# Kernel optimization log

Hardware: AMD Instinct MI355X
Metric: run time of the kernel (lower is better)

Reference implementation:

```python
import jax, jax.numpy as jnp
import numpy as np

B, T, N_IN, N_H, N_OUT = 128, 1024, 512, 1024, 256


def setup_inputs() -> dict:
    key = jax.random.key(0)
    ks = jax.random.split(key, 14)
    s_in = 1.0 / np.sqrt(N_IN)
    s_h = 1.0 / np.sqrt(N_H)
    d = {
        'u': jax.random.normal(ks[0], (B, T, N_IN), jnp.float32),
        'W_uf': jax.random.normal(ks[1], (N_IN, N_H), jnp.float32) * s_in,
        'W_ui': jax.random.normal(ks[2], (N_IN, N_H), jnp.float32) * s_in,
        'W_uo': jax.random.normal(ks[3], (N_IN, N_H), jnp.float32) * s_in,
        'W_uc': jax.random.normal(ks[4], (N_IN, N_H), jnp.float32) * s_in,
        'W_hf': jax.random.normal(ks[5], (N_H, N_H), jnp.float32) * s_h,
        'W_hi': jax.random.normal(ks[6], (N_H, N_H), jnp.float32) * s_h,
        'W_ho': jax.random.normal(ks[7], (N_H, N_H), jnp.float32) * s_h,
        'W_hc': jax.random.normal(ks[8], (N_H, N_H), jnp.float32) * s_h,
        'W_hy': jax.random.normal(ks[9], (N_H, N_OUT), jnp.float32) * s_h,
        'b_f': jnp.zeros((N_H,), jnp.float32),
        'b_i': jnp.zeros((N_H,), jnp.float32),
        'b_o': jnp.zeros((N_H,), jnp.float32),
        'b_c': jnp.zeros((N_H,), jnp.float32),
        'b_y': jnp.zeros((N_OUT,), jnp.float32),
        'h0': jax.random.normal(ks[10], (N_H,), jnp.float32),
        'c0': jax.random.normal(ks[11], (N_H,), jnp.float32),
    }
    return d


def _lstm_forward(u, W_uf, W_ui, W_uo, W_uc, W_hf, W_hi, W_ho, W_hc, W_hy,
                  b_f, b_i, b_o, b_c, b_y, h0, c0):
    Bsz = u.shape[0]
    # Precompute all input-driven gate pre-activations as one batched GEMM per gate.
    xf = jnp.einsum('btn,nh->bth', u, W_uf) + b_f
    xi = jnp.einsum('btn,nh->bth', u, W_ui) + b_i
    xo = jnp.einsum('btn,nh->bth', u, W_uo) + b_o
    xc = jnp.einsum('btn,nh->bth', u, W_uc) + b_c
    xs = jnp.stack([xf, xi, xo, xc], axis=0)  # [4, B, T, H]
    xs = jnp.moveaxis(xs, 2, 0)               # [T, 4, B, H]

    h = jnp.broadcast_to(h0, (Bsz, h0.shape[0]))
    c = jnp.broadcast_to(c0, (Bsz, c0.shape[0]))

    def step(carry, x_t):
        h, c = carry
        f = jax.nn.sigmoid(h @ W_hf + x_t[0])
        i = jax.nn.sigmoid(h @ W_hi + x_t[1])
        o = jax.nn.sigmoid(h @ W_ho + x_t[2])
        c_tilde = jnp.tanh(h @ W_hc + x_t[3])
        # NOTE: faithful to source: c = f * h + i * c_tilde (uses h, not c)
        c_new = f * h + i * c_tilde
        h_new = o * jnp.tanh(c_new)
        y_t = jax.nn.softmax(h_new @ W_hy + b_y, axis=1)
        return (h_new, c_new), y_t

    (_, _), ys = jax.lax.scan(step, (h, c), xs)  # ys: [T, B, N_out]
    return jnp.swapaxes(ys, 0, 1)                # [B, T, N_out]


def reference(u, W_uf, W_ui, W_uo, W_uc, W_hf, W_hi, W_ho, W_hc, W_hy,
              b_f, b_i, b_o, b_c, b_y, h0, c0):
    return _lstm_forward(u, W_uf, W_ui, W_uo, W_uc, W_hf, W_hi, W_ho, W_hc,
                         W_hy, b_f, b_i, b_o, b_c, b_y, h0, c0)
```

## Files before the change

### kernel.cpp

```cpp
#include <hip/hip_runtime.h>
#include <hip/hip_bf16.h>
#include <hip/hip_cooperative_groups.h>

namespace cg = cooperative_groups;

#define BDIM 128
#define TDIM 1024
#define NIN  512
#define NH   1024
#define NOUT 256
#define NITER (TDIM + 2)

__device__ __forceinline__ float sigmoidf_(float x) { return 1.f / (1.f + __expf(-x)); }

struct ScanArgs {
    const float* u;
    const float* Wu[4];
    const float* Wh[4];
    const float* WhyT;
    const float* bg[4];
    const float* by;
    float* hb0; float* hb1;
    float* lg0; float* lg1;
    float* out;
};

__device__ __forceinline__ void scan_iter(const ScanArgs& A, int it,
                                          float* pre, float* ylds)
{
    const int tid  = threadIdx.x;
    const int bx   = blockIdx.x;
    const int lane = tid & 63;
    const int wv   = tid >> 6;
    const int ks   = lane & 7;
    const int cgi  = (lane >> 3) & 3;
    const int rg   = wv * 2 + (lane >> 5);
    const int c0   = bx * 4;

    const float* hcur = (it & 1) ? A.hb1 : A.hb0;
    float* hnext      = (it & 1) ? A.hb0 : A.hb1;
    float* Lw         = (it & 1) ? A.lg1 : A.lg0;
    const float* Lr   = (it & 1) ? A.lg0 : A.lg1;

    if (it >= 2 && bx < BDIM && tid < 64) {
        const int r = bx, t = it - 2;
        float4 v = *(const float4*)(Lr + (size_t)r * NOUT + tid * 4);
        float mx = fmaxf(fmaxf(v.x, v.y), fmaxf(v.z, v.w));
#pragma unroll
        for (int d = 1; d < 64; d <<= 1) mx = fmaxf(mx, __shfl_xor(mx, d));
        v.x = __expf(v.x - mx); v.y = __expf(v.y - mx);
        v.z = __expf(v.z - mx); v.w = __expf(v.w - mx);
        float s = v.x + v.y + v.z + v.w;
#pragma unroll
        for (int d = 1; d < 64; d <<= 1) s += __shfl_xor(s, d);
        const float inv = 1.f / s;
        v.x *= inv; v.y *= inv; v.z *= inv; v.w *= inv;
        *(float4*)(A.out + ((size_t)r * TDIM + t) * NOUT + tid * 4) = v;
    }

    if (it < TDIM) {
        const int t  = it;
        const int r0 = rg * 8;
        const float* Wu = A.Wu[cgi] + c0;
        const float* Wh = A.Wh[cgi] + c0;
        float acc[8][4];
#pragma unroll
        for (int i = 0; i < 8; ++i)
#pragma unroll
            for (int j = 0; j < 4; ++j) acc[i][j] = 0.f;

        {
            const int kb = ks * 64;
#pragma unroll 2
            for (int q = 0; q < 16; ++q) {
                const int k = kb + q * 4;
                const float4 w0 = *(const float4*)(Wu + (size_t)(k + 0) * NH);
                const float4 w1 = *(const float4*)(Wu + (size_t)(k + 1) * NH);
                const float4 w2 = *(const float4*)(Wu + (size_t)(k + 2) * NH);
                const float4 w3 = *(const float4*)(Wu + (size_t)(k + 3) * NH);
#pragma unroll
                for (int i = 0; i < 8; ++i) {
                    const float4 a = *(const float4*)(A.u +
                        ((size_t)(r0 + i) * TDIM + t) * NIN + k);
                    acc[i][0] = fmaf(a.x, w0.x, acc[i][0]);
                    acc[i][1] = fmaf(a.x, w0.y, acc[i][1]);
                    acc[i][2] = fmaf(a.x, w0.z, acc[i][2]);
                    acc[i][3] = fmaf(a.x, w0.w, acc[i][3]);
                    acc[i][0] = fmaf(a.y, w1.x, acc[i][0]);
                    acc[i][1] = fmaf(a.y, w1.y, acc[i][1]);
                    acc[i][2] = fmaf(a.y, w1.z, acc[i][2]);
                    acc[i][3] = fmaf(a.y, w1.w, acc[i][3]);
                    acc[i][0] = fmaf(a.z, w2.x, acc[i][0]);
                    acc[i][1] = fmaf(a.z, w2.y, acc[i][1]);
                    acc[i][2] = fmaf(a.z, w2.z, acc[i][2]);
                    acc[i][3] = fmaf(a.z, w2.w, acc[i][3]);
                    acc[i][0] = fmaf(a.w, w3.x, acc[i][0]);
                    acc[i][1] = fmaf(a.w, w3.y, acc[i][1]);
                    acc[i][2] = fmaf(a.w, w3.z, acc[i][2]);
                    acc[i][3] = fmaf(a.w, w3.w, acc[i][3]);
                }
            }
        }
        {
            const int kb = ks * 128;
#pragma unroll 2
            for (int q = 0; q < 32; ++q) {
                const int k = kb + q * 4;
                const float4 w0 = *(const float4*)(Wh + (size_t)(k + 0) * NH);
                const float4 w1 = *(const float4*)(Wh + (size_t)(k + 1) * NH);
                const float4 w2 = *(const float4*)(Wh + (size_t)(k + 2) * NH);
                const float4 w3 = *(const float4*)(Wh + (size_t)(k + 3) * NH);
#pragma unroll
                for (int i = 0; i < 8; ++i) {
                    const float4 a = *(const float4*)(hcur +
                        (size_t)(r0 + i) * NH + k);
                    acc[i][0] = fmaf(a.x, w0.x, acc[i][0]);
                    acc[i][1] = fmaf(a.x, w0.y, acc[i][1]);
                    acc[i][2] = fmaf(a.x, w0.z, acc[i][2]);
                    acc[i][3] = fmaf(a.x, w0.w, acc[i][3]);
                    acc[i][0] = fmaf(a.y, w1.x, acc[i][0]);
                    acc[i][1] = fmaf(a.y, w1.y, acc[i][1]);
                    acc[i][2] = fmaf(a.y, w1.z, acc[i][2]);
                    acc[i][3] = fmaf(a.y, w1.w, acc[i][3]);
                    acc[i][0] = fmaf(a.z, w2.x, acc[i][0]);
                    acc[i][1] = fmaf(a.z, w2.y, acc[i][1]);
                    acc[i][2] = fmaf(a.z, w2.z, acc[i][2]);
                    acc[i][3] = fmaf(a.z, w2.w, acc[i][3]);
                    acc[i][0] = fmaf(a.w, w3.x, acc[i][0]);
                    acc[i][1] = fmaf(a.w, w3.y, acc[i][1]);
                    acc[i][2] = fmaf(a.w, w3.z, acc[i][2]);
                    acc[i][3] = fmaf(a.w, w3.w, acc[i][3]);
                }
            }
        }
#pragma unroll
        for (int i = 0; i < 8; ++i)
#pragma unroll
            for (int j = 0; j < 4; ++j) {
                float v = acc[i][j];
                v += __shfl_xor(v, 1);
                v += __shfl_xor(v, 2);
                v += __shfl_xor(v, 4);
                acc[i][j] = v;
            }
        if (ks == 0) {
#pragma unroll
            for (int i = 0; i < 8; ++i)
                *(float4*)&pre[(size_t)(r0 + i) * 20 + cgi * 4] =
                    make_float4(acc[i][0], acc[i][1], acc[i][2], acc[i][3]);
        }
    }

    if (it >= 1 && it <= TDIM) {
        const int yrow = tid >> 2;
        const int kb   = (tid & 3) * 256;
        const float* hp = hcur + (size_t)yrow * NH;
        const float* wp = A.WhyT + (size_t)bx * NH;
        float ya = 0.f;
#pragma unroll 4
        for (int q = 0; q < 64; ++q) {
            const int k = kb + q * 4;
            const float4 h4 = *(const float4*)(hp + k);
            const float4 w4 = *(const float4*)(wp + k);
            ya = fmaf(h4.x, w4.x, ya);
            ya = fmaf(h4.y, w4.y, ya);
            ya = fmaf(h4.z, w4.z, ya);
            ya = fmaf(h4.w, w4.w, ya);
        }
        ylds[tid] = ya;
    }

    __syncthreads();

    if (it < TDIM) {
        const int row = tid >> 2, hc = tid & 3;
        const float* pr = pre + (size_t)row * 20 + hc;
        const float gf = sigmoidf_(pr[0]  + A.bg[0][c0 + hc]);
        const float gi = sigmoidf_(pr[4]  + A.bg[1][c0 + hc]);
        const float go = sigmoidf_(pr[8]  + A.bg[2][c0 + hc]);
        const float ct = tanhf    (pr[12] + A.bg[3][c0 + hc]);
        const float ho = hcur[(size_t)row * NH + c0 + hc];
        const float cn = gf * ho + gi * ct;
        hnext[(size_t)row * NH + c0 + hc] = go * tanhf(cn);
    }

    if (it >= 1 && it <= TDIM && tid < BDIM) {
        const float4 yv = *(const float4*)&ylds[tid * 4];
        Lw[(size_t)tid * NOUT + bx] = yv.x + yv.y + yv.z + yv.w + A.by[bx];
    }
}

__global__ __launch_bounds__(512, 2) void scan_coop(ScanArgs A)
{
    __shared__ float pre[BDIM * 20];
    __shared__ float ylds[512];
    cg::grid_group grid = cg::this_grid();
    for (int it = 0; it < NITER; ++it) {
        scan_iter(A, it, pre, ylds);
        grid.sync();
    }
}

__global__ __launch_bounds__(512, 2) void scan_step(ScanArgs A, int it)
{
    __shared__ float pre[BDIM * 20];
    __shared__ float ylds[512];
    scan_iter(A, it, pre, ylds);
}

__global__ void transpose_why(const float* __restrict__ Why,
                              float* __restrict__ WhyT)
{
    __shared__ float tile[32][33];
    const int k0 = blockIdx.x * 32;
    const int n0 = blockIdx.y * 32;
    const int tx = threadIdx.x, ty = threadIdx.y;
#pragma unroll
    for (int r = 0; r < 4; ++r)
        tile[ty * 4 + r][tx] = Why[(size_t)(k0 + ty * 4 + r) * NOUT + n0 + tx];
    __syncthreads();
#pragma unroll
    for (int r = 0; r < 4; ++r)
        WhyT[(size_t)(n0 + ty * 4 + r) * NH + k0 + tx] = tile[tx][ty * 4 + r];
}

__global__ void init_h(const float* __restrict__ h0, float* __restrict__ hb)
{
    const int i = blockIdx.x * 256 + threadIdx.x;
    hb[i] = h0[i & (NH - 1)];
}

extern "C" void kernel_launch(void* const* d_in, const int* in_sizes, int n_in,
                              void* d_out, int out_size, void* d_ws, size_t ws_size,
                              hipStream_t stream)
{
    (void)in_sizes; (void)n_in; (void)out_size; (void)ws_size;
    const float* u   = (const float*)d_in[0];
    const float* Wuf = (const float*)d_in[1];
    const float* Wui = (const float*)d_in[2];
    const float* Wuo = (const float*)d_in[3];
    const float* Wuc = (const float*)d_in[4];
    const float* Whf = (const float*)d_in[5];
    const float* Whi = (const float*)d_in[6];
    const float* Who = (const float*)d_in[7];
    const float* Whc = (const float*)d_in[8];
    const float* Why = (const float*)d_in[9];
    const float* bf  = (const float*)d_in[10];
    const float* bi  = (const float*)d_in[11];
    const float* bo  = (const float*)d_in[12];
    const float* bc  = (const float*)d_in[13];
    const float* by  = (const float*)d_in[14];
    const float* h0  = (const float*)d_in[15];
    float* out = (float*)d_out;

    float* WhyT = (float*)d_ws;
    float* hb0  = WhyT + (size_t)NOUT * NH;
    float* hb1  = hb0  + (size_t)BDIM * NH;
    float* lg0  = hb1  + (size_t)BDIM * NH;
    float* lg1  = lg0  + (size_t)BDIM * NOUT;

    transpose_why<<<dim3(NH / 32, NOUT / 32), dim3(32, 8), 0, stream>>>(Why, WhyT);
    init_h<<<dim3(BDIM * NH / 256), dim3(256), 0, stream>>>(h0, hb0);

    ScanArgs A;
    A.u = u;
    A.Wu[0] = Wuf; A.Wu[1] = Wui; A.Wu[2] = Wuo; A.Wu[3] = Wuc;
    A.Wh[0] = Whf; A.Wh[1] = Whi; A.Wh[2] = Who; A.Wh[3] = Whc;
    A.WhyT = WhyT;
    A.bg[0] = bf; A.bg[1] = bi; A.bg[2] = bo; A.bg[3] = bc;
    A.by = by;
    A.hb0 = hb0; A.hb1 = hb1; A.lg0 = lg0; A.lg1 = lg1;
    A.out = out;

    void* args[] = { (void*)&A };
    hipError_t e = hipLaunchCooperativeKernel((void*)scan_coop, dim3(256),
                                              dim3(512), args, 0, stream);
    if (e != hipSuccess) {
        for (int it = 0; it < NITER; ++it)
            scan_step<<<dim3(256), dim3(512), 0, stream>>>(A, it);
    }
}
```

Measured before the change: 209.9 ms.

## Pack gate weights per column block and double threads per block in scan

A new pre-pass packs the four input and four recurrent gate weight matrices into one contiguous array per 4-column slice. Each block's weight reads then become a single contiguous stream instead of strided rows from eight matrices. The scan kernel now runs 1024 threads per block, each handling 4 batch rows instead of 8, and remaps blocks to columns with a swizzle. The output projection is redistributed across the first 128 blocks and reduced with shuffles instead of shared memory, and softmax moves to the other 128 blocks. This adds a large workspace requirement and a fallback path if it is missing; the 1024-thread launch bounds may limit registers.

```diff
diff --git a/kernel.cpp b/kernel.cpp
--- a/kernel.cpp
+++ b/kernel.cpp
@@ -9,6 +9,7 @@
 #define NIN  512
 #define NH   1024
 #define NOUT 256
+#define KTOT (NIN + NH)
 #define NITER (TDIM + 2)
 
 __device__ __forceinline__ float sigmoidf_(float x) { return 1.f / (1.f + __expf(-x)); }
@@ -17,6 +18,7 @@
     const float* u;
     const float* Wu[4];
     const float* Wh[4];
+    const float* Wpack;
     const float* WhyT;
     const float* bg[4];
     const float* by;
@@ -25,8 +27,8 @@
     float* out;
 };
 
-__device__ __forceinline__ void scan_iter(const ScanArgs& A, int it,
-                                          float* pre, float* ylds)
+template <bool PACKED>
+__device__ __forceinline__ void scan_iter(const ScanArgs& A, int it, float* pre)
 {
     const int tid  = threadIdx.x;
     const int bx   = blockIdx.x;
@@ -35,15 +37,16 @@
     const int ks   = lane & 7;
     const int cgi  = (lane >> 3) & 3;
     const int rg   = wv * 2 + (lane >> 5);
-    const int c0   = bx * 4;
+    const int cc   = (bx & 7) * 32 + (bx >> 3);
+    const int c0   = cc * 4;
 
     const float* hcur = (it & 1) ? A.hb1 : A.hb0;
     float* hnext      = (it & 1) ? A.hb0 : A.hb1;
     float* Lw         = (it & 1) ? A.lg1 : A.lg0;
     const float* Lr   = (it & 1) ? A.lg0 : A.lg1;
 
-    if (it >= 2 && bx < BDIM && tid < 64) {
-        const int r = bx, t = it - 2;
+    if (it >= 2 && bx >= 128 && tid < 64) {
+        const int r = bx - 128, t = it - 2;
         float4 v = *(const float4*)(Lr + (size_t)r * NOUT + tid * 4);
         float mx = fmaxf(fmaxf(v.x, v.y), fmaxf(v.z, v.w));
 #pragma unroll
@@ -60,81 +63,151 @@
 
     if (it < TDIM) {
         const int t  = it;
-        const int r0 = rg * 8;
-        const float* Wu = A.Wu[cgi] + c0;
-        const float* Wh = A.Wh[cgi] + c0;
-        float acc[8][4];
-#pragma unroll
-        for (int i = 0; i < 8; ++i)
+        const int r0 = rg * 4;
+        float acc[4][4];
+#pragma unroll
+        for (int i = 0; i < 4; ++i)
 #pragma unroll
             for (int j = 0; j < 4; ++j) acc[i][j] = 0.f;
 
-        {
-            const int kb = ks * 64;
+        if (PACKED) {
+            const float* pk = A.Wpack + ((size_t)cc * KTOT) * 16 + cgi * 4;
+            {
+                const float* pku = pk + (size_t)(ks * 64) * 16;
+                const float* up  = A.u + (size_t)t * NIN + (size_t)ks * 64;
 #pragma unroll 2
-            for (int q = 0; q < 16; ++q) {
-                const int k = kb + q * 4;
-                const float4 w0 = *(const float4*)(Wu + (size_t)(k + 0) * NH);
-                const float4 w1 = *(const float4*)(Wu + (size_t)(k + 1) * NH);
-                const float4 w2 = *(const float4*)(Wu + (size_t)(k + 2) * NH);
-                const float4 w3 = *(const float4*)(Wu + (size_t)(k + 3) * NH);
-#pragma unroll
-                for (int i = 0; i < 8; ++i) {
-                    const float4 a = *(const float4*)(A.u +
-                        ((size_t)(r0 + i) * TDIM + t) * NIN + k);
-                    acc[i][0] = fmaf(a.x, w0.x, acc[i][0]);
-                    acc[i][1] = fmaf(a.x, w0.y, acc[i][1]);
-                    acc[i][2] = fmaf(a.x, w0.z, acc[i][2]);
-                    acc[i][3] = fmaf(a.x, w0.w, acc[i][3]);
-                    acc[i][0] = fmaf(a.y, w1.x, acc[i][0]);
-                    acc[i][1] = fmaf(a.y, w1.y, acc[i][1]);
-                    acc[i][2] = fmaf(a.y, w1.z, acc[i][2]);
-                    acc[i][3] = fmaf(a.y, w1.w, acc[i][3]);
-                    acc[i][0] = fmaf(a.z, w2.x, acc[i][0]);
-                    acc[i][1] = fmaf(a.z, w2.y, acc[i][1]);
-                    acc[i][2] = fmaf(a.z, w2.z, acc[i][2]);
-                    acc[i][3] = fmaf(a.z, w2.w, acc[i][3]);
-                    acc[i][0] = fmaf(a.w, w3.x, acc[i][0]);
-                    acc[i][1] = fmaf(a.w, w3.y, acc[i][1]);
-                    acc[i][2] = fmaf(a.w, w3.z, acc[i][2]);
-                    acc[i][3] = fmaf(a.w, w3.w, acc[i][3]);
+                for (int q = 0; q < 16; ++q) {
+                    const int k4 = q * 4;
+                    const float4 w0 = *(const float4*)(pku + (k4 + 0) * 16);
+                    const float4 w1 = *(const float4*)(pku + (k4 + 1) * 16);
+                    const float4 w2 = *(const float4*)(pku + (k4 + 2) * 16);
+                    const float4 w3 = *(const float4*)(pku + (k4 + 3) * 16);
+#pragma unroll
+                    for (int i = 0; i < 4; ++i) {
+                        const float4 a = *(const float4*)(up +
+                            (size_t)(r0 + i) * TDIM * NIN + k4);
+                        acc[i][0] = fmaf(a.x, w0.x, acc[i][0]);
+                        acc[i][1] = fmaf(a.x, w0.y, acc[i][1]);
+                        acc[i][2] = fmaf(a.x, w0.z, acc[i][2]);
+                        acc[i][3] = fmaf(a.x, w0.w, acc[i][3]);
+                        acc[i][0] = fmaf(a.y, w1.x, acc[i][0]);
+                        acc[i][1] = fmaf(a.y, w1.y, acc[i][1]);
+                        acc[i][2] = fmaf(a.y, w1.z, acc[i][2]);
+                        acc[i][3] = fmaf(a.y, w1.w, acc[i][3]);
+                        acc[i][0] = fmaf(a.z, w2.x, acc[i][0]);
+                        acc[i][1] = fmaf(a.z, w2.y, acc[i][1]);
+                        acc[i][2] = fmaf(a.z, w2.z, acc[i][2]);
+                        acc[i][3] = fmaf(a.z, w2.w, acc[i][3]);
+                        acc[i][0] = fmaf(a.w, w3.x, acc[i][0]);
+                        acc[i][1] = fmaf(a.w, w3.y, acc[i][1]);
+                        acc[i][2] = fmaf(a.w, w3.z, acc[i][2]);
+                        acc[i][3] = fmaf(a.w, w3.w, acc[i][3]);
+                    }
                 }
             }
-        }
-        {
-            const int kb = ks * 128;
+            {
+                const float* pkh = pk + (size_t)(NIN + ks * 128) * 16;
+                const float* hp  = hcur + (size_t)ks * 128;
 #pragma unroll 2
-            for (int q = 0; q < 32; ++q) {
-                const int k = kb + q * 4;
-                const float4 w0 = *(const float4*)(Wh + (size_t)(k + 0) * NH);
-                const float4 w1 = *(const float4*)(Wh + (size_t)(k + 1) * NH);
-                const float4 w2 = *(const float4*)(Wh + (size_t)(k + 2) * NH);
-                const float4 w3 = *(const float4*)(Wh + (size_t)(k + 3) * NH);
-#pragma unroll
-                for (int i = 0; i < 8; ++i) {
-                    const float4 a = *(const float4*)(hcur +
-                        (size_t)(r0 + i) * NH + k);
-                    acc[i][0] = fmaf(a.x, w0.x, acc[i][0]);
-                    acc[i][1] = fmaf(a.x, w0.y, acc[i][1]);
-                    acc[i][2] = fmaf(a.x, w0.z, acc[i][2]);
-                    acc[i][3] = fmaf(a.x, w0.w, acc[i][3]);
-                    acc[i][0] = fmaf(a.y, w1.x, acc[i][0]);
-                    acc[i][1] = fmaf(a.y, w1.y, acc[i][1]);
-                    acc[i][2] = fmaf(a.y, w1.z, acc[i][2]);
-                    acc[i][3] = fmaf(a.y, w1.w, acc[i][3]);
-                    acc[i][0] = fmaf(a.z, w2.x, acc[i][0]);
-                    acc[i][1] = fmaf(a.z, w2.y, acc[i][1]);
-                    acc[i][2] = fmaf(a.z, w2.z, acc[i][2]);
-                    acc[i][3] = fmaf(a.z, w2.w, acc[i][3]);
-                    acc[i][0] = fmaf(a.w, w3.x, acc[i][0]);
-                    acc[i][1] = fmaf(a.w, w3.y, acc[i][1]);
-                    acc[i][2] = fmaf(a.w, w3.z, acc[i][2]);
-                    acc[i][3] = fmaf(a.w, w3.w, acc[i][3]);
+                for (int q = 0; q < 32; ++q) {
+                    const int k4 = q * 4;
+                    const float4 w0 = *(const float4*)(pkh + (k4 + 0) * 16);
+                    const float4 w1 = *(const float4*)(pkh + (k4 + 1) * 16);
+                    const float4 w2 = *(const float4*)(pkh + (k4 + 2) * 16);
+                    const float4 w3 = *(const float4*)(pkh + (k4 + 3) * 16);
+#pragma unroll
+                    for (int i = 0; i < 4; ++i) {
+                        const float4 a = *(const float4*)(hp +
+                            (size_t)(r0 + i) * NH + k4);
+                        acc[i][0] = fmaf(a.x, w0.x, acc[i][0]);
+                        acc[i][1] = fmaf(a.x, w0.y, acc[i][1]);
+                        acc[i][2] = fmaf(a.x, w0.z, acc[i][2]);
+                        acc[i][3] = fmaf(a.x, w0.w, acc[i][3]);
+                        acc[i][0] = fmaf(a.y, w1.x, acc[i][0]);
+                        acc[i][1] = fmaf(a.y, w1.y, acc[i][1]);
+                        acc[i][2] = fmaf(a.y, w1.z, acc[i][2]);
+                        acc[i][3] = fmaf(a.y, w1.w, acc[i][3]);
+                        acc[i][0] = fmaf(a.z, w2.x, acc[i][0]);
+                        acc[i][1] = fmaf(a.z, w2.y, acc[i][1]);
+                        acc[i][2] = fmaf(a.z, w2.z, acc[i][2]);
+                        acc[i][3] = fmaf(a.z, w2.w, acc[i][3]);
+                        acc[i][0] = fmaf(a.w, w3.x, acc[i][0]);
+                        acc[i][1] = fmaf(a.w, w3.y, acc[i][1]);
+                        acc[i][2] = fmaf(a.w, w3.z, acc[i][2]);
+                        acc[i][3] = fmaf(a.w, w3.w, acc[i][3]);
+                    }
                 }
             }
-        }
-#pragma unroll
-        for (int i = 0; i < 8; ++i)
+        } else {
+            const float* Wu = A.Wu[cgi] + c0;
+            const float* Wh = A.Wh[cgi] + c0;
+            {
+                const int kb = ks * 64;
+#pragma unroll 2
+                for (int q = 0; q < 16; ++q) {
+                    const int k = kb + q * 4;
+                    const float4 w0 = *(const float4*)(Wu + (size_t)(k + 0) * NH);
+                    const float4 w1 = *(const float4*)(Wu + (size_t)(k + 1) * NH);
+                    const float4 w2 = *(const float4*)(Wu + (size_t)(k + 2) * NH);
+                    const float4 w3 = *(const float4*)(Wu + (size_t)(k + 3) * NH);
+#pragma unroll
+                    for (int i = 0; i < 4; ++i) {
+                        const float4 a = *(const float4*)(A.u +
+                            ((size_t)(r0 + i) * TDIM + t) * NIN + k);
+                        acc[i][0] = fmaf(a.x, w0.x, acc[i][0]);
+                        acc[i][1] = fmaf(a.x, w0.y, acc[i][1]);
+                        acc[i][2] = fmaf(a.x, w0.z, acc[i][2]);
+                        acc[i][3] = fmaf(a.x, w0.w, acc[i][3]);
+                        acc[i][0] = fmaf(a.y, w1.x, acc[i][0]);
+                        acc[i][1] = fmaf(a.y, w1.y, acc[i][1]);
+                        acc[i][2] = fmaf(a.y, w1.z, acc[i][2]);
+                        acc[i][3] = fmaf(a.y, w1.w, acc[i][3]);
+                        acc[i][0] = fmaf(a.z, w2.x, acc[i][0]);
+                        acc[i][1] = fmaf(a.z, w2.y, acc[i][1]);
+                        acc[i][2] = fmaf(a.z, w2.z, acc[i][2]);
+                        acc[i][3] = fmaf(a.z, w2.w, acc[i][3]);
+                        acc[i][0] = fmaf(a.w, w3.x, acc[i][0]);
+                        acc[i][1] = fmaf(a.w, w3.y, acc[i][1]);
+                        acc[i][2] = fmaf(a.w, w3.z, acc[i][2]);
+                        acc[i][3] = fmaf(a.w, w3.w, acc[i][3]);
+                    }
+                }
+            }
+            {
+                const int kb = ks * 128;
+#pragma unroll 2
+                for (int q = 0; q < 32; ++q) {
+                    const int k = kb + q * 4;
+                    const float4 w0 = *(const float4*)(Wh + (size_t)(k + 0) * NH);
+                    const float4 w1 = *(const float4*)(Wh + (size_t)(k + 1) * NH);
+                    const float4 w2 = *(const float4*)(Wh + (size_t)(k + 2) * NH);
+                    const float4 w3 = *(const float4*)(Wh + (size_t)(k + 3) * NH);
+#pragma unroll
+                    for (int i = 0; i < 4; ++i) {
+                        const float4 a = *(const float4*)(hcur +
+                            (size_t)(r0 + i) * NH + k);
+                        acc[i][0] = fmaf(a.x, w0.x, acc[i][0]);
+                        acc[i][1] = fmaf(a.x, w0.y, acc[i][1]);
+                        acc[i][2] = fmaf(a.x, w0.z, acc[i][2]);
+                        acc[i][3] = fmaf(a.x, w0.w, acc[i][3]);
+                        acc[i][0] = fmaf(a.y, w1.x, acc[i][0]);
+                        acc[i][1] = fmaf(a.y, w1.y, acc[i][1]);
+                        acc[i][2] = fmaf(a.y, w1.z, acc[i][2]);
+                        acc[i][3] = fmaf(a.y, w1.w, acc[i][3]);
+                        acc[i][0] = fmaf(a.z, w2.x, acc[i][0]);
+                        acc[i][1] = fmaf(a.z, w2.y, acc[i][1]);
+                        acc[i][2] = fmaf(a.z, w2.z, acc[i][2]);
+                        acc[i][3] = fmaf(a.z, w2.w, acc[i][3]);
+                        acc[i][0] = fmaf(a.w, w3.x, acc[i][0]);
+                        acc[i][1] = fmaf(a.w, w3.y, acc[i][1]);
+                        acc[i][2] = fmaf(a.w, w3.z, acc[i][2]);
+                        acc[i][3] = fmaf(a.w, w3.w, acc[i][3]);
+                    }
+                }
+            }
+        }
+#pragma unroll
+        for (int i = 0; i < 4; ++i)
 #pragma unroll
             for (int j = 0; j < 4; ++j) {
                 float v = acc[i][j];
@@ -145,34 +218,36 @@
             }
         if (ks == 0) {
 #pragma unroll
-            for (int i = 0; i < 8; ++i)
+            for (int i = 0; i < 4; ++i)
                 *(float4*)&pre[(size_t)(r0 + i) * 20 + cgi * 4] =
                     make_float4(acc[i][0], acc[i][1], acc[i][2], acc[i][3]);
         }
     }
 
-    if (it >= 1 && it <= TDIM) {
-        const int yrow = tid >> 2;
-        const int kb   = (tid & 3) * 256;
-        const float* hp = hcur + (size_t)yrow * NH;
-        const float* wp = A.WhyT + (size_t)bx * NH;
+    if (it >= 1 && it <= TDIM && bx < 128) {
+        const int r  = (bx & 1) * 64 + (tid >> 4);
+        const int c  = ((bx >> 1) << 2) + ((tid >> 2) & 3);
+        const int kb = (tid & 3) * 256;
+        const float* hp = hcur + (size_t)r * NH + kb;
+        const float* wp = A.WhyT + (size_t)c * NH + kb;
         float ya = 0.f;
 #pragma unroll 4
         for (int q = 0; q < 64; ++q) {
-            const int k = kb + q * 4;
-            const float4 h4 = *(const float4*)(hp + k);
-            const float4 w4 = *(const float4*)(wp + k);
+            const float4 h4 = *(const float4*)(hp + q * 4);
+            const float4 w4 = *(const float4*)(wp + q * 4);
             ya = fmaf(h4.x, w4.x, ya);
             ya = fmaf(h4.y, w4.y, ya);
             ya = fmaf(h4.z, w4.z, ya);
             ya = fmaf(h4.w, w4.w, ya);
         }
-        ylds[tid] = ya;
+        ya += __shfl_xor(ya, 1);
+        ya += __shfl_xor(ya, 2);
+        if ((tid & 3) == 0) Lw[(size_t)r * NOUT + c] = ya + A.by[c];
     }
 
     __syncthreads();
 
-    if (it < TDIM) {
+    if (it < TDIM && tid < 512) {
         const int row = tid >> 2, hc = tid & 3;
         const float* pr = pre + (size_t)row * 20 + hc;
         const float gf = sigmoidf_(pr[0]  + A.bg[0][c0 + hc]);
@@ -183,29 +258,47 @@
         const float cn = gf * ho + gi * ct;
         hnext[(size_t)row * NH + c0 + hc] = go * tanhf(cn);
     }
-
-    if (it >= 1 && it <= TDIM && tid < BDIM) {
-        const float4 yv = *(const float4*)&ylds[tid * 4];
-        Lw[(size_t)tid * NOUT + bx] = yv.x + yv.y + yv.z + yv.w + A.by[bx];
-    }
-}
-
-__global__ __launch_bounds__(512, 2) void scan_coop(ScanArgs A)
+}
+
+template <bool PACKED>
+__global__ __launch_bounds__(1024, 4) void scan_coop(ScanArgs A)
 {
     __shared__ float pre[BDIM * 20];
-    __shared__ float ylds[512];
     cg::grid_group grid = cg::this_grid();
     for (int it = 0; it < NITER; ++it) {
-        scan_iter(A, it, pre, ylds);
+        scan_iter<PACKED>(A, it, pre);
         grid.sync();
     }
 }
 
-__global__ __launch_bounds__(512, 2) void scan_step(ScanArgs A, int it)
+template <bool PACKED>
+__global__ __launch_bounds__(1024, 4) void scan_step(ScanArgs A, int it)
 {
     __shared__ float pre[BDIM * 20];
-    __shared__ float ylds[512];
-    scan_iter(A, it, pre, ylds);
+    scan_iter<PACKED>(A, it, pre);
+}
+
+__global__ void pack_weights(
+    const float* __restrict__ Wuf, const float* __restrict__ Wui,
+    const float* __restrict__ Wuo, const float* __restrict__ Wuc,
+    const float* __restrict__ Whf, const float* __restrict__ Whi,
+    const float* __restrict__ Who, const float* __restrict__ Whc,
+    float* __restrict__ Wpack)
+{
+    const int cc = blockIdx.x;
+    const int c0 = cc * 4;
+    const float* Wu[4] = {Wuf, Wui, Wuo, Wuc};
+    const float* Wh[4] = {Whf, Whi, Who, Whc};
+    for (int k = threadIdx.x; k < KTOT; k += 256) {
+        float4* dst = (float4*)(Wpack + ((size_t)cc * KTOT + k) * 16);
+#pragma unroll
+        for (int g = 0; g < 4; ++g) {
+            const float* src = (k < NIN)
+                ? (Wu[g] + (size_t)k * NH + c0)
+                : (Wh[g] + (size_t)(k - NIN) * NH + c0);
+            dst[g] = *(const float4*)src;
+        }
+    }
 }
 
 __global__ void transpose_why(const float* __restrict__ Why,
@@ -234,7 +327,7 @@
                               void* d_out, int out_size, void* d_ws, size_t ws_size,
                               hipStream_t stream)
 {
-    (void)in_sizes; (void)n_in; (void)out_size; (void)ws_size;
+    (void)in_sizes; (void)n_in; (void)out_size;
     const float* u   = (const float*)d_in[0];
     const float* Wuf = (const float*)d_in[1];
     const float* Wui = (const float*)d_in[2];
@@ -258,25 +351,43 @@
     float* hb1  = hb0  + (size_t)BDIM * NH;
     float* lg0  = hb1  + (size_t)BDIM * NH;
     float* lg1  = lg0  + (size_t)BDIM * NOUT;
+    float* Wpk  = lg1  + (size_t)BDIM * NOUT;
+
+    const size_t smallElems = (size_t)NOUT * NH + 2 * (size_t)BDIM * NH
+                            + 2 * (size_t)BDIM * NOUT;
+    const size_t packElems  = (size_t)256 * KTOT * 16;
+    const bool usePack = ws_size >= (smallElems + packElems) * sizeof(float);
 
     transpose_why<<<dim3(NH / 32, NOUT / 32), dim3(32, 8), 0, stream>>>(Why, WhyT);
     init_h<<<dim3(BDIM * NH / 256), dim3(256), 0, stream>>>(h0, hb0);
+    if (usePack)
+        pack_weights<<<dim3(256), dim3(256), 0, stream>>>(
+            Wuf, Wui, Wuo, Wuc, Whf, Whi, Who, Whc, Wpk);
 
     ScanArgs A;
     A.u = u;
     A.Wu[0] = Wuf; A.Wu[1] = Wui; A.Wu[2] = Wuo; A.Wu[3] = Wuc;
     A.Wh[0] = Whf; A.Wh[1] = Whi; A.Wh[2] = Who; A.Wh[3] = Whc;
-    A.WhyT = WhyT;
+    A.Wpack = Wpk; A.WhyT = WhyT;
     A.bg[0] = bf; A.bg[1] = bi; A.bg[2] = bo; A.bg[3] = bc;
     A.by = by;
     A.hb0 = hb0; A.hb1 = hb1; A.lg0 = lg0; A.lg1 = lg1;
     A.out = out;
 
     void* args[] = { (void*)&A };
-    hipError_t e = hipLaunchCooperativeKernel((void*)scan_coop, dim3(256),
-                                              dim3(512), args, 0, stream);
+    hipError_t e;
+    if (usePack)
+        e = hipLaunchCooperativeKernel((void*)scan_coop<true>, dim3(256),
+                                       dim3(1024), args, 0, stream);
+    else
+        e = hipLaunchCooperativeKernel((void*)scan_coop<false>, dim3(256),
+                                       dim3(1024), args, 0, stream);
     if (e != hipSuccess) {
-        for (int it = 0; it < NITER; ++it)
-            scan_step<<<dim3(256), dim3(512), 0, stream>>>(A, it);
-    }
-}
+        for (int it = 0; it < NITER; ++it) {
+            if (usePack)
+                scan_step<true><<<dim3(256), dim3(1024), 0, stream>>>(A, it);
+            else
+                scan_step<false><<<dim3(256), dim3(1024), 0, stream>>>(A, it);
+        }
+    }
+}
```

After: 262.7 ms. +25.2%, slower.
